# Performance work log

Measured on AMD Instinct MI355X. Metric: run time of the kernel, lower is better.

## Reference

```python
import jax, jax.numpy as jnp
import numpy as np

N = 10000        # nodes
E = 160000       # active edges
NS = 128         # scalar (0e) channels per tensor
NV = 64          # vector (1o) channels per tensor
LAT = 64         # latent dim
AVG_NEIGH = 16.0
SQ2 = float(np.sqrt(2.0))
SQ3 = float(np.sqrt(3.0))
EPS = 1e-5


def setup_inputs() -> dict:
    key = jax.random.key(0)
    ks = jax.random.split(key, 24)
    rn = lambda k, s: jax.random.normal(k, s, jnp.float32)
    d = {}
    d["latents"] = rn(ks[0], (E, LAT))
    d["node_features"] = rn(ks[1], (N, NS + 3 * NV))
    d["edge_features"] = rn(ks[2], (E, NS + 3 * NV))
    d["edge_sh"] = rn(ks[3], (E, 4))
    d["edge_index"] = jax.random.randint(ks[4], (2, E), 0, N)
    d["atom_type"] = jax.random.randint(ks[5], (N,), 0, 10)
    d["active_edges"] = jnp.arange(E)
    # separable layer norm affine params (node and edge)
    d["g_s_n"] = jnp.ones((NS,), jnp.float32); d["b_s_n"] = jnp.zeros((NS,), jnp.float32)
    d["g_v_n"] = jnp.ones((NV,), jnp.float32)
    d["g_s_e"] = jnp.ones((NS,), jnp.float32); d["b_s_e"] = jnp.zeros((NS,), jnp.float32)
    d["g_v_e"] = jnp.ones((NV,), jnp.float32)
    # FullyConnectedTensorProduct weights (path-normalized init).
    # tp input: 2*NS scalars, 2*NV vectors; sh: 1 scalar + 1 vector;
    # tp output: NS+NV scalars (scalars+gates), NV vectors.
    nSt, nVt, nSo = 2 * NS, 2 * NV, NS + NV
    d["W_ss0"] = rn(ks[6], (nSt, nSo)) / np.sqrt(nSt * 2)
    d["W_vv0"] = rn(ks[7], (nVt, nSo)) / np.sqrt(nVt * 2)
    d["W_sv1"] = rn(ks[8], (nSt, NV)) / np.sqrt(nSt * 3)
    d["W_vs1"] = rn(ks[9], (nVt, NV)) / np.sqrt(nVt * 3)
    d["W_vv1"] = rn(ks[10], (nVt, NV)) / np.sqrt(nVt * 3)
    # lin_post (per-l channel mixing)
    d["Wp_s"] = rn(ks[11], (NS, NS)) / np.sqrt(NS)
    d["Wp_v"] = rn(ks[12], (NV, NV)) / np.sqrt(NV)
    # env_embed_mlps: single linear latent -> weight_numel (NS+NV channels)
    d["W_env"] = rn(ks[13], (LAT, NS + NV)) / np.sqrt(LAT)
    # linear_res
    d["Wr_s"] = rn(ks[14], (NS, NS)) / np.sqrt(NS)
    d["Wr_v"] = rn(ks[15], (NV, NV)) / np.sqrt(NV)
    return d


def _sep_ln(x, g_s, b_s, g_v):
    # separable layer norm: standard LN on scalars, RMS-of-norms on vectors
    s = x[:, :NS]
    v = x[:, NS:].reshape(-1, NV, 3)
    mu = s.mean(-1, keepdims=True)
    var = ((s - mu) ** 2).mean(-1, keepdims=True)
    s = (s - mu) * jax.lax.rsqrt(var + EPS) * g_s + b_s
    vn = jnp.mean(jnp.sum(v * v, -1), -1, keepdims=True)  # (B,1)
    v = v * jax.lax.rsqrt(vn + EPS)[:, :, None] * g_v[None, :, None]
    return s, v


def _forward(latents, node_features, edge_features, edge_sh, edge_index,
             atom_type, active_edges,
             g_s_n, b_s_n, g_v_n, g_s_e, b_s_e, g_v_e,
             W_ss0, W_vv0, W_sv1, W_vs1, W_vv1,
             Wp_s, Wp_v, W_env, Wr_s, Wr_v):
    ec = edge_index[0][active_edges]                      # (E,) center nodes
    ns, nv = _sep_ln(node_features, g_s_n, b_s_n, g_v_n)
    es, ev = _sep_ln(edge_features, g_s_e, b_s_e, g_v_e)
    S = jnp.concatenate([ns[ec], es], axis=-1)            # (E, 2*NS)
    V = jnp.concatenate([nv[ec], ev], axis=1)             # (E, 2*NV, 3)
    sh0 = edge_sh[:, :1]                                  # (E,1)
    sh1 = edge_sh[:, 1:]                                  # (E,3)
    # fully-connected tensor product (tp_in x sh -> gate input)
    dotV = jnp.einsum('ecd,ed->ec', V, sh1) / SQ3         # 1x1->0
    out0 = (S * sh0) @ W_ss0 + dotV @ W_vv0               # (E, NS+NV) scalars
    out_v = (S @ W_sv1)[:, :, None] * sh1[:, None, :]     # 0x1->1
    out_v = out_v + jnp.einsum('ecd,cf->efd', V, W_vs1) * sh0[:, :, None]  # 1x0->1
    cross = jnp.cross(V, sh1[:, None, :]) / SQ2           # 1x1->1
    out_v = out_v + jnp.einsum('ecd,cf->efd', cross, W_vv1)  # (E, NV, 3)
    # gate
    s = jax.nn.silu(out0[:, :NS])
    gates = jax.nn.sigmoid(out0[:, NS:])
    v = out_v * gates[:, :, None]
    # lin_post
    s = s @ Wp_s
    v = jnp.einsum('ecd,cf->efd', v, Wp_v)
    # env weights from latents (elementwise linear per channel)
    w = latents[active_edges] @ W_env                     # (E, NS+NV)
    s = s * w[:, :NS]
    v = v * w[:, NS:][:, :, None]
    msg = jnp.concatenate([s, v.reshape(-1, 3 * NV)], axis=-1)  # (E, 320)
    agg = jax.ops.segment_sum(msg, ec, num_segments=N)
    agg = agg * jnp.float32(1.0 / np.sqrt(AVG_NEIGH))
    # residual linear on raw node features
    rs = node_features[:, :NS] @ Wr_s
    rv = jnp.einsum('ncd,cf->nfd', node_features[:, NS:].reshape(-1, NV, 3), Wr_v)
    res = jnp.concatenate([rs, rv.reshape(-1, 3 * NV)], axis=-1)
    return res + agg


def reference(latents, node_features, edge_features, edge_sh, edge_index,
              atom_type, active_edges,
              g_s_n, b_s_n, g_v_n, g_s_e, b_s_e, g_v_e,
              W_ss0, W_vv0, W_sv1, W_vs1, W_vv1,
              Wp_s, Wp_v, W_env, Wr_s, Wr_v):
    return _forward(latents, node_features, edge_features, edge_sh, edge_index,
                    atom_type, active_edges,
                    g_s_n, b_s_n, g_v_n, g_s_e, b_s_e, g_v_e,
                    W_ss0, W_vv0, W_sv1, W_vs1, W_vv1,
                    Wp_s, Wp_v, W_env, Wr_s, Wr_v)
```

## Files before the change

kernel.cpp:

```cpp
#include <hip/hip_runtime.h>

#define N_NODES 10000
#define N_EDGES 160000
#define NSC 128
#define ROW 320
#define EPS_LN 1e-5f
#define INV_SQ2 0.70710678118654752440f
#define INV_SQ3 0.57735026918962576451f

typedef unsigned short bfraw;
typedef __attribute__((ext_vector_type(8))) short short8;
typedef __attribute__((ext_vector_type(4))) float float4x;
typedef __attribute__((ext_vector_type(2))) float float2x;

__device__ __forceinline__ float bf2f(bfraw u) {
    union { unsigned int i; float f; } x; x.i = ((unsigned int)u) << 16; return x.f;
}
__device__ __forceinline__ bfraw f2bf(float f) {
    union { float f; unsigned int i; } x; x.f = f;
    unsigned int i = x.i;
    unsigned int lsb = (i >> 16) & 1u;
    i += 0x7fffu + lsb;
    return (bfraw)(i >> 16);
}
__device__ __forceinline__ unsigned cvt_pk_bf16(float lo, float hi) {
    unsigned r;
    asm("v_cvt_pk_bf16_f32 %0, %1, %2" : "=v"(r) : "v"(lo), "v"(hi));
    return r;
}
template<bool B> __device__ __forceinline__ float LD(const void* p, size_t i) {
    if (B) return bf2f(((const bfraw*)p)[i]);
    else   return ((const float*)p)[i];
}
template<bool B> __device__ __forceinline__ void ST(void* p, size_t i, float v) {
    if (B) ((bfraw*)p)[i] = f2bf(v);
    else   ((float*)p)[i] = v;
}
template<bool B> __device__ __forceinline__ float2x LD2(const void* p, size_t i) {
    float2x r;
    if (B) {
        unsigned u = *(const unsigned*)((const bfraw*)p + i);
        r.x = bf2f((bfraw)(u & 0xffffu)); r.y = bf2f((bfraw)(u >> 16));
    } else {
        r = *(const float2x*)((const float*)p + i);
    }
    return r;
}
template<bool B> __device__ __forceinline__ float4x LD4(const void* p, size_t i) {
    float4x r;
    if (B) {
        unsigned long long u = *(const unsigned long long*)((const bfraw*)p + i);
        r.x = bf2f((bfraw)(u & 0xffffu));
        r.y = bf2f((bfraw)((u >> 16) & 0xffffu));
        r.z = bf2f((bfraw)((u >> 32) & 0xffffu));
        r.w = bf2f((bfraw)(u >> 48));
    } else {
        r = *(const float4x*)((const float*)p + i);
    }
    return r;
}
__device__ __forceinline__ float wred64(float v) {
#pragma unroll
    for (int o = 32; o > 0; o >>= 1) v += __shfl_xor(v, o, 64);
    return v;
}
__device__ __forceinline__ void wredx12(float a[12]) {
#pragma unroll
    for (int o = 32; o > 0; o >>= 1) {
        float t[12];
#pragma unroll
        for (int i = 0; i < 12; i++) t[i] = __shfl_xor(a[i], o, 64);
#pragma unroll
        for (int i = 0; i < 12; i++) a[i] += t[i];
    }
}
__device__ __forceinline__ float silu_f(float x) { return x / (1.0f + __expf(-x)); }
__device__ __forceinline__ float sigm_f(float x) { return 1.0f / (1.0f + __expf(-x)); }

#define MFMA16(a, b, c) __builtin_amdgcn_mfma_f32_16x16x32_bf16((a), (b), (c), 0, 0, 0)

__device__ __forceinline__ int SDI(int r, int c) { return r * 384 + (c ^ ((r & 7) << 3)); }
__device__ __forceinline__ int X64(int r, int c) { return r * 64  + (c ^ ((r & 7) << 3)); }
__device__ __forceinline__ int SPI(int r, int c) { return r * 128 + (c ^ ((r & 7) << 3)); }
__device__ __forceinline__ int WVI(int r, int c) { return r * 192 + (c ^ ((r & 7) << 2)); }

__device__ __forceinline__ int dtype_flag(const void* g_s_n) {
    return (((const unsigned int*)g_s_n)[0] == 0x3F803F80u) ? 1 : 0;
}

__device__ __forceinline__ void pack_body(int idx, int fl,
    const void* Wss0, const void* Wvv0, const void* Wsv1, const void* Wvs1,
    const void* Wvv1, const void* Wps,  const void* Wpv,  const void* Wenv,
    const void* Wrs,  const void* Wrv,  bfraw* __restrict__ dst)
{
    const void* src; int K, N, base;
    if      (idx <  49152) { src = Wss0; K = 256; N = 192; base = 0; }
    else if (idx <  73728) { src = Wvv0; K = 128; N = 192; base = 49152; }
    else if (idx <  90112) { src = Wsv1; K = 256; N =  64; base = 73728; }
    else if (idx <  98304) { src = Wvs1; K = 128; N =  64; base = 90112; }
    else if (idx < 106496) { src = Wvv1; K = 128; N =  64; base = 98304; }
    else if (idx < 122880) { src = Wps;  K = 128; N = 128; base = 106496; }
    else if (idx < 126976) { src = Wpv;  K =  64; N =  64; base = 122880; }
    else if (idx < 139264) { src = Wenv; K =  64; N = 192; base = 126976; }
    else if (idx < 155648) { src = Wrs;  K = 128; N = 128; base = 139264; }
    else                   { src = Wrv;  K =  64; N =  64; base = 155648; }
    int li = idx - base;
    int j = li & 7, l = (li >> 3) & 63, t = li >> 9;
    int NT = N >> 4;
    int nt = t % NT, kt = t / NT;
    int k = kt * 32 + ((l >> 4) << 3) + j;
    int n = (nt << 4) + (l & 15);
    float v = fl ? bf2f(((const bfraw*)src)[(size_t)k * N + n])
                 : ((const float*)src)[(size_t)k * N + n];
    dst[idx] = f2bf(v);
}

template<bool B>
__device__ __forceinline__ void node_ln_body(int n, int lane,
    const void* nf, const void* g_s, const void* b_s, const void* g_v,
    bfraw* __restrict__ nsnv)
{
    size_t base = (size_t)n * ROW;
    float2x s = LD2<B>(nf, base + 2 * lane);
    float mu = wred64(s.x + s.y) * (1.0f / 128.0f);
    float m2 = wred64(s.x * s.x + s.y * s.y) * (1.0f / 128.0f);
    float rs = rsqrtf(m2 - mu * mu + EPS_LN);
    float2x g = LD2<B>(g_s, 2 * lane), b = LD2<B>(b_s, 2 * lane);
    float o0 = (s.x - mu) * rs * g.x + b.x;
    float o1 = (s.y - mu) * rs * g.y + b.y;
    float vx = LD<B>(nf, base + NSC + 3 * lane);
    float vy = LD<B>(nf, base + NSC + 3 * lane + 1);
    float vz = LD<B>(nf, base + NSC + 3 * lane + 2);
    float vn = wred64(vx * vx + vy * vy + vz * vz) * (1.0f / 64.0f);
    float rv = rsqrtf(vn + EPS_LN) * LD<B>(g_v, lane);
    bfraw* row = nsnv + (size_t)n * 320;
    ((unsigned*)row)[lane] = cvt_pk_bf16(o0, o1);
    row[128 + lane] = f2bf(vx * rv);
    row[192 + lane] = f2bf(vy * rv);
    row[256 + lane] = f2bf(vz * rv);
}

__global__ __launch_bounds__(256) void prep_k(
    const void* Wss0, const void* Wvv0, const void* Wsv1, const void* Wvs1,
    const void* Wvv1, const void* Wps,  const void* Wpv,  const void* Wenv,
    const void* Wrs,  const void* Wrv,  bfraw* __restrict__ pk,
    const int* __restrict__ eidx, const int* __restrict__ act, int* __restrict__ counts,
    const void* nf, const void* g_s_n, const void* b_s_n, const void* g_v_n,
    bfraw* __restrict__ nsnv)
{
    int fl = dtype_flag(g_s_n);
    int idx = blockIdx.x * 256 + threadIdx.x;
    if (idx < 159744)
        pack_body(idx, fl, Wss0, Wvv0, Wsv1, Wvs1, Wvv1, Wps, Wpv, Wenv, Wrs, Wrv, pk);
    if (idx < N_EDGES)
        atomicAdd(&counts[eidx[act[idx]]], 1);
    int w = threadIdx.x >> 6, lane = threadIdx.x & 63;
    int n = blockIdx.x * 4 + w;
    if (fl) node_ln_body<true >(n, lane, nf, g_s_n, b_s_n, g_v_n, nsnv);
    else    node_ln_body<false>(n, lane, nf, g_s_n, b_s_n, g_v_n, nsnv);
}

__global__ __launch_bounds__(1024) void scan_k(const int* __restrict__ counts,
                                               int* __restrict__ starts) {
    __shared__ int wsum[16];
    int t = threadIdx.x;
    int lo = t * 10;
    int lanev = t & 63, wv = t >> 6;
    int c[10];
    int s = 0;
    if (lo < N_NODES) {
#pragma unroll
        for (int j = 0; j < 10; j++) { c[j] = counts[lo + j]; s += c[j]; }
    }
    int ps = s;
#pragma unroll
    for (int o = 1; o < 64; o <<= 1) {
        int u = __shfl_up(ps, o, 64);
        if (lanev >= o) ps += u;
    }
    if (lanev == 63) wsum[wv] = ps;
    __syncthreads();
    if (t == 0) {
        int acc = 0;
#pragma unroll
        for (int i = 0; i < 16; i++) { int v = wsum[i]; wsum[i] = acc; acc += v; }
        starts[N_NODES] = acc;
    }
    __syncthreads();
    if (lo < N_NODES) {
        int acc = wsum[wv] + ps - s;
#pragma unroll
        for (int j = 0; j < 10; j++) { starts[lo + j] = acc; acc += c[j]; }
    }
}

__global__ void fill_k(const int* __restrict__ eidx, const int* __restrict__ act,
                       const int* __restrict__ starts, int* __restrict__ cursor,
                       int* __restrict__ inv) {
    int e = blockIdx.x * 256 + threadIdx.x;
    if (e < N_EDGES) {
        int n = eidx[act[e]];
        int pos = atomicAdd(&cursor[n], 1);
        inv[e] = starts[n] + pos;
    }
}

template<bool B>
__device__ void edge_body(char* smem, int tid,
    const bfraw* __restrict__ nsnv,
    const void* ef, const void* esh,
    const int* __restrict__ eidx, const int* __restrict__ act,
    const int* __restrict__ inv,
    const void* lat,
    const void* g_s_e, const void* b_s_e, const void* g_v_e,
    const bfraw* __restrict__ pk,
    bfraw* __restrict__ msg)
{
    bfraw* SD     = (bfraw*)(smem);
    bfraw* Vn     = (bfraw*)(smem + 12288);
    bfraw* Ve     = (bfraw*)(smem + 18432);
    bfraw* gate_u = (bfraw*)(smem + 18432);
    bfraw* sp_u   = (bfraw*)(smem + 20480);
    bfraw* lat_u  = (bfraw*)(smem + 24576);
    float* sh_f   = (float*)(smem + 26624);
    int*   slot_s = (int*)(smem + 26880);
    float* wenv_f = (float*)(smem);

    const bfraw* pWss0 = pk;
    const bfraw* pWvv0 = pk + 49152;
    const bfraw* pWsv1 = pk + 73728;
    const bfraw* pWvs1 = pk + 90112;
    const bfraw* pWvv1 = pk + 98304;
    const bfraw* pWps  = pk + 106496;
    const bfraw* pWpv  = pk + 122880;
    const bfraw* pWenv = pk + 126976;

    const int w = tid >> 6, lane = tid & 63;
    const int nl = lane & 15, mq = lane >> 4;
    const int e0 = blockIdx.x * 16;

    float2x gse = LD2<B>(g_s_e, 2 * lane), bse = LD2<B>(b_s_e, 2 * lane);
    float gve  = LD<B>(g_v_e, lane);

    int ae_[4], cn_[4], sl_[4];
#pragma unroll
    for (int i = 0; i < 4; i++) { ae_[i] = act[e0 + w * 4 + i]; sl_[i] = inv[e0 + w * 4 + i]; }
#pragma unroll
    for (int i = 0; i < 4; i++) cn_[i] = eidx[ae_[i]];

    float es0[4], es1[4], ex[4], ey[4], ez[4];
    float shv[4][4];
#pragma unroll
    for (int i = 0; i < 4; i++) {
        int el = w * 4 + i, e = e0 + el;
        float4x sh = LD4<B>(esh, (size_t)e * 4);
        shv[i][0] = sh.x; shv[i][1] = sh.y; shv[i][2] = sh.z; shv[i][3] = sh.w;
        size_t eb = (size_t)e * ROW;
        float2x es = LD2<B>(ef, eb + 2 * lane);
        es0[i] = es.x; es1[i] = es.y;
        ex[i]  = LD<B>(ef, eb + NSC + 3 * lane);
        ey[i]  = LD<B>(ef, eb + NSC + 3 * lane + 1);
        ez[i]  = LD<B>(ef, eb + NSC + 3 * lane + 2);
        const bfraw* nr = nsnv + (size_t)cn_[i] * 320;
        unsigned nsp = ((const unsigned*)nr)[lane];
        bfraw nvx = nr[128 + lane], nvy = nr[192 + lane], nvz = nr[256 + lane];
        float nx = bf2f(nvx), ny = bf2f(nvy), nz = bf2f(nvz);
        *(unsigned*)&SD[SDI(el, 2 * lane)] = nsp;
        SD[SDI(el, 256 + lane)] = f2bf((nx * sh.y + ny * sh.z + nz * sh.w) * INV_SQ3);
        Vn[X64(el, lane)]      = nvx;
        Vn[X64(16 + el, lane)] = nvy;
        Vn[X64(32 + el, lane)] = nvz;
        if (lane < 32) {
            float2x la = LD2<B>(lat, (size_t)ae_[i] * 64 + 2 * lane);
            *(unsigned*)&lat_u[X64(el, 2 * lane)] = cvt_pk_bf16(la.x, la.y);
        }
        if (lane == 0) {
            sh_f[el * 4]     = sh.x; sh_f[el * 4 + 1] = sh.y;
            sh_f[el * 4 + 2] = sh.z; sh_f[el * 4 + 3] = sh.w;
            slot_s[el] = sl_[i];
        }
    }
    float red[12];
#pragma unroll
    for (int i = 0; i < 4; i++) {
        red[i]     = es0[i] + es1[i];
        red[4 + i] = es0[i] * es0[i] + es1[i] * es1[i];
        red[8 + i] = ex[i] * ex[i] + ey[i] * ey[i] + ez[i] * ez[i];
    }
    wredx12(red);
#pragma unroll
    for (int i = 0; i < 4; i++) {
        int el = w * 4 + i;
        float mu  = red[i] * (1.0f / 128.0f);
        float var = red[4 + i] * (1.0f / 128.0f) - mu * mu;
        float rs  = rsqrtf(var + EPS_LN);
        float o0  = (es0[i] - mu) * rs * gse.x + bse.x;
        float o1  = (es1[i] - mu) * rs * gse.y + bse.y;
        float rv  = rsqrtf(red[8 + i] * (1.0f / 64.0f) + EPS_LN) * gve;
        float exn = ex[i] * rv, eyn = ey[i] * rv, ezn = ez[i] * rv;
        *(unsigned*)&SD[SDI(el, 128 + 2 * lane)] = cvt_pk_bf16(o0, o1);
        SD[SDI(el, 320 + lane)] = f2bf((exn * shv[i][1] + eyn * shv[i][2] + ezn * shv[i][3]) * INV_SQ3);
        Ve[X64(el, lane)]       = f2bf(exn);
        Ve[X64(16 + el, lane)]  = f2bf(eyn);
        Ve[X64(32 + el, lane)]  = f2bf(ezn);
    }
    __syncthreads();

    float4x sA0={0,0,0,0}, sA1={0,0,0,0}, sA2={0,0,0,0}, cSV={0,0,0,0};
    {
        const bfraw* ps = pWss0 + (size_t)(3 * w * 64 + lane) * 8;
        const bfraw* pv = pWsv1 + (size_t)(w * 64 + lane) * 8;
        short8 b0[4], b1[4];
#define LDG1(kt, D) do { \
        D[0] = *(const short8*)(ps + (kt) * 6144);        \
        D[1] = *(const short8*)(ps + (kt) * 6144 + 512);  \
        D[2] = *(const short8*)(ps + (kt) * 6144 + 1024); \
        D[3] = *(const short8*)(pv + (kt) * 2048); } while (0)
        LDG1(0, b0); LDG1(1, b1);
#pragma unroll
        for (int kt = 0; kt < 8; kt++) {
            short8 a = *(const short8*)&SD[SDI(nl, kt * 32 + mq * 8)];
            if ((kt & 1) == 0) {
                sA0 = MFMA16(a, b0[0], sA0); sA1 = MFMA16(a, b0[1], sA1);
                sA2 = MFMA16(a, b0[2], sA2); cSV = MFMA16(a, b0[3], cSV);
                if (kt + 2 < 8) LDG1(kt + 2, b0);
            } else {
                sA0 = MFMA16(a, b1[0], sA0); sA1 = MFMA16(a, b1[1], sA1);
                sA2 = MFMA16(a, b1[2], sA2); cSV = MFMA16(a, b1[3], cSV);
                if (kt + 2 < 8) LDG1(kt + 2, b1);
            }
        }
#undef LDG1
    }
    float4x dA0={0,0,0,0}, dA1={0,0,0,0}, dA2={0,0,0,0};
    {
        const bfraw* pd = pWvv0 + (size_t)(3 * w * 64 + lane) * 8;
        short8 c0[3], c1[3];
#define LDGD(kt, D) do { \
        D[0] = *(const short8*)(pd + (kt) * 6144);        \
        D[1] = *(const short8*)(pd + (kt) * 6144 + 512);  \
        D[2] = *(const short8*)(pd + (kt) * 6144 + 1024); } while (0)
        LDGD(0, c0); LDGD(1, c1);
#pragma unroll
        for (int kt = 0; kt < 4; kt++) {
            short8 a = *(const short8*)&SD[SDI(nl, 256 + kt * 32 + mq * 8)];
            if ((kt & 1) == 0) {
                dA0 = MFMA16(a, c0[0], dA0); dA1 = MFMA16(a, c0[1], dA1); dA2 = MFMA16(a, c0[2], dA2);
                if (kt + 2 < 4) LDGD(kt + 2, c0);
            } else {
                dA0 = MFMA16(a, c1[0], dA0); dA1 = MFMA16(a, c1[1], dA1); dA2 = MFMA16(a, c1[2], dA2);
                if (kt + 2 < 4) LDGD(kt + 2, c1);
            }
        }
#undef LDGD
    }
    float o_g1[3][4];
#pragma unroll
    for (int r = 0; r < 4; r++) {
        float sh0 = sh_f[(mq * 4 + r) * 4];
        o_g1[0][r] = sh0 * sA0[r] + dA0[r];
        o_g1[1][r] = sh0 * sA1[r] + dA1[r];
        o_g1[2][r] = sh0 * sA2[r] + dA2[r];
    }
    float4x H[3] = {{0,0,0,0},{0,0,0,0},{0,0,0,0}};
    float4x K[3] = {{0,0,0,0},{0,0,0,0},{0,0,0,0}};
    {
        const bfraw* ph = pWvs1 + (size_t)(w * 64 + lane) * 8;
        const bfraw* pq = pWvv1 + (size_t)(w * 64 + lane) * 8;
        short8 gH0 = *(const short8*)(ph);
        short8 gH1 = *(const short8*)(ph + 2048);
        short8 gH2 = *(const short8*)(ph + 4096);
        short8 gH3 = *(const short8*)(ph + 6144);
        short8 gK0 = *(const short8*)(pq);
        short8 gK1 = *(const short8*)(pq + 2048);
        short8 gK2 = *(const short8*)(pq + 4096);
        short8 gK3 = *(const short8*)(pq + 6144);
#pragma unroll
        for (int d = 0; d < 3; d++) {
            short8 a0 = *(const short8*)&Vn[X64(d * 16 + nl, mq * 8)];
            short8 a1 = *(const short8*)&Vn[X64(d * 16 + nl, 32 + mq * 8)];
            short8 a2 = *(const short8*)&Ve[X64(d * 16 + nl, mq * 8)];
            short8 a3 = *(const short8*)&Ve[X64(d * 16 + nl, 32 + mq * 8)];
            H[d] = MFMA16(a0, gH0, H[d]); K[d] = MFMA16(a0, gK0, K[d]);
            H[d] = MFMA16(a1, gH1, H[d]); K[d] = MFMA16(a1, gK1, K[d]);
            H[d] = MFMA16(a2, gH2, H[d]); K[d] = MFMA16(a2, gK2, K[d]);
            H[d] = MFMA16(a3, gH3, H[d]); K[d] = MFMA16(a3, gK3, K[d]);
        }
    }
    __syncthreads();

#pragma unroll
    for (int t = 0; t < 3; t++) {
        int tile = 3 * w + t;
#pragma unroll
        for (int r = 0; r < 4; r++) {
            int el = mq * 4 + r;
            float o = o_g1[t][r];
            if (tile < 8) sp_u[SPI(el, tile * 16 + nl)]         = f2bf(silu_f(o));
            else          gate_u[X64(el, (tile - 8) * 16 + nl)] = f2bf(sigm_f(o));
        }
    }
    __syncthreads();

    {
        int f = w * 16 + nl;
#pragma unroll
        for (int r = 0; r < 4; r++) {
            int el = mq * 4 + r;
            float g   = bf2f(gate_u[X64(el, f)]);
            float svv = cSV[r];
            float s0v = sh_f[el * 4], b0 = sh_f[el * 4 + 1], b1 = sh_f[el * 4 + 2], b2 = sh_f[el * 4 + 3];
            float ov0 = svv * b0 + s0v * H[0][r] + (b2 * K[1][r] - b1 * K[2][r]) * INV_SQ2;
            float ov1 = svv * b1 + s0v * H[1][r] + (b0 * K[2][r] - b2 * K[0][r]) * INV_SQ2;
            float ov2 = svv * b2 + s0v * H[2][r] + (b1 * K[0][r] - b0 * K[1][r]) * INV_SQ2;
            Vn[X64(el, f)]      = f2bf(ov0 * g);
            Vn[X64(16 + el, f)] = f2bf(ov1 * g);
            Vn[X64(32 + el, f)] = f2bf(ov2 * g);
        }
    }
    __syncthreads();

    float4x s2_0 = {0,0,0,0}, s2_1 = {0,0,0,0};
    {
        const bfraw* pp = pWps + (size_t)(w * 64 + lane) * 8;
        short8 u0[2], u1[2];
#define LDS2(kt, D) do { \
        D[0] = *(const short8*)(pp + (kt) * 4096);         \
        D[1] = *(const short8*)(pp + (kt) * 4096 + 2048); } while (0)
        LDS2(0, u0); LDS2(1, u1);
#pragma unroll
        for (int kt = 0; kt < 4; kt++) {
            short8 a = *(const short8*)&sp_u[SPI(nl, kt * 32 + mq * 8)];
            if ((kt & 1) == 0) {
                s2_0 = MFMA16(a, u0[0], s2_0); s2_1 = MFMA16(a, u0[1], s2_1);
                if (kt + 2 < 4) LDS2(kt + 2, u0);
            } else {
                s2_0 = MFMA16(a, u1[0], s2_0); s2_1 = MFMA16(a, u1[1], s2_1);
                if (kt + 2 < 4) LDS2(kt + 2, u1);
            }
        }
#undef LDS2
    }
    float4x wv0 = {0,0,0,0}, wv1 = {0,0,0,0}, wv2 = {0,0,0,0};
    {
        const bfraw* pe = pWenv + (size_t)(3 * w * 64 + lane) * 8;
        short8 e00 = *(const short8*)(pe);
        short8 e01 = *(const short8*)(pe + 512);
        short8 e02 = *(const short8*)(pe + 1024);
        short8 e10 = *(const short8*)(pe + 6144);
        short8 e11 = *(const short8*)(pe + 6144 + 512);
        short8 e12 = *(const short8*)(pe + 6144 + 1024);
        short8 a0 = *(const short8*)&lat_u[X64(nl, mq * 8)];
        short8 a1 = *(const short8*)&lat_u[X64(nl, 32 + mq * 8)];
        wv0 = MFMA16(a0, e00, wv0); wv0 = MFMA16(a1, e10, wv0);
        wv1 = MFMA16(a0, e01, wv1); wv1 = MFMA16(a1, e11, wv1);
        wv2 = MFMA16(a0, e02, wv2); wv2 = MFMA16(a1, e12, wv2);
    }
    float4x v2[3] = {{0,0,0,0},{0,0,0,0},{0,0,0,0}};
    {
        const bfraw* pz = pWpv + (size_t)(w * 64 + lane) * 8;
        short8 z0 = *(const short8*)(pz);
        short8 z1 = *(const short8*)(pz + 2048);
#pragma unroll
        for (int d = 0; d < 3; d++) {
            short8 a0 = *(const short8*)&Vn[X64(d * 16 + nl, mq * 8)];
            short8 a1 = *(const short8*)&Vn[X64(d * 16 + nl, 32 + mq * 8)];
            v2[d] = MFMA16(a0, z0, v2[d]);
            v2[d] = MFMA16(a1, z1, v2[d]);
        }
    }
    {
        float4x wvv[3] = {wv0, wv1, wv2};
#pragma unroll
        for (int t = 0; t < 3; t++)
#pragma unroll
            for (int r = 0; r < 4; r++)
                wenv_f[WVI(mq * 4 + r, (3 * w + t) * 16 + nl)] = wvv[t][r];
    }
    __syncthreads();

    int mslot[4];
#pragma unroll
    for (int r = 0; r < 4; r++) mslot[r] = slot_s[mq * 4 + r];
#pragma unroll
    for (int t = 0; t < 2; t++) {
        int c = (w + 4 * t) * 16 + nl;
        float4x s2v = (t == 0) ? s2_0 : s2_1;
#pragma unroll
        for (int r = 0; r < 4; r++) {
            int el = mq * 4 + r;
            msg[(size_t)mslot[r] * 320 + c] = f2bf(s2v[r] * wenv_f[WVI(el, c)]);
        }
    }
    {
        int f = w * 16 + nl;
#pragma unroll
        for (int r = 0; r < 4; r++) {
            int el = mq * 4 + r;
            float we = wenv_f[WVI(el, 128 + f)];
            size_t base = (size_t)mslot[r] * 320 + NSC + 3 * f;
            msg[base]     = f2bf(v2[0][r] * we);
            msg[base + 1] = f2bf(v2[1][r] * we);
            msg[base + 2] = f2bf(v2[2][r] * we);
        }
    }
}

__global__ __launch_bounds__(256, 6) void edge_mfma_k(
    const bfraw* __restrict__ nsnv,
    const void* ef, const void* esh,
    const int* __restrict__ eidx, const int* __restrict__ act,
    const int* __restrict__ inv,
    const void* lat,
    const void* g_s_e, const void* b_s_e, const void* g_v_e,
    const bfraw* __restrict__ pk,
    bfraw* __restrict__ msg, const void* g_s_n)
{
    __shared__ __align__(16) char smem[26944];
    if (dtype_flag(g_s_n))
        edge_body<true >(smem, threadIdx.x, nsnv, ef, esh, eidx, act, inv, lat,
                         g_s_e, b_s_e, g_v_e, pk, msg);
    else
        edge_body<false>(smem, threadIdx.x, nsnv, ef, esh, eidx, act, inv, lat,
                         g_s_e, b_s_e, g_v_e, pk, msg);
}

__device__ __forceinline__ float lo16(unsigned u) { return bf2f((bfraw)(u & 0xffffu)); }
__device__ __forceinline__ float hi16(unsigned u) { return bf2f((bfraw)(u >> 16)); }

__global__ __launch_bounds__(256) void gather_k(
    const bfraw* __restrict__ msg, const int* __restrict__ starts,
    float* __restrict__ agg)
{
    int w = threadIdx.x >> 6, lane = threadIdx.x & 63;
    int n = blockIdx.x * 4 + w;
    if (n >= N_NODES) return;
    int s0 = starts[n], s1 = starts[n + 1];
    bool half = lane < 32;
    float l0 = 0, h0 = 0, l1 = 0, h1 = 0, l2 = 0, h2 = 0;
    const unsigned* p = (const unsigned*)msg + (size_t)s0 * 160;
    int cnt = s1 - s0;
    int i = 0;
    for (; i + 3 < cnt; i += 4) {
        const unsigned* r0 = p + (size_t)i * 160;
        const unsigned* r1 = r0 + 160;
        const unsigned* r2 = r0 + 320;
        const unsigned* r3 = r0 + 480;
        unsigned a0 = r0[lane], b0 = r0[64 + lane];
        unsigned a1 = r1[lane], b1 = r1[64 + lane];
        unsigned a2 = r2[lane], b2 = r2[64 + lane];
        unsigned a3 = r3[lane], b3 = r3[64 + lane];
        unsigned c0 = half ? r0[128 + lane] : 0u;
        unsigned c1 = half ? r1[128 + lane] : 0u;
        unsigned c2 = half ? r2[128 + lane] : 0u;
        unsigned c3 = half ? r3[128 + lane] : 0u;
        l0 += (lo16(a0) + lo16(a1)) + (lo16(a2) + lo16(a3));
        h0 += (hi16(a0) + hi16(a1)) + (hi16(a2) + hi16(a3));
        l1 += (lo16(b0) + lo16(b1)) + (lo16(b2) + lo16(b3));
        h1 += (hi16(b0) + hi16(b1)) + (hi16(b2) + hi16(b3));
        l2 += (lo16(c0) + lo16(c1)) + (lo16(c2) + lo16(c3));
        h2 += (hi16(c0) + hi16(c1)) + (hi16(c2) + hi16(c3));
    }
    for (; i < cnt; i++) {
        const unsigned* r = p + (size_t)i * 160;
        unsigned a = r[lane], b = r[64 + lane];
        unsigned c = half ? r[128 + lane] : 0u;
        l0 += lo16(a); h0 += hi16(a);
        l1 += lo16(b); h1 += hi16(b);
        l2 += lo16(c); h2 += hi16(c);
    }
    float* o = agg + (size_t)n * ROW;
    float2x v0 = {l0, h0}, v1 = {l1, h1}, v2 = {l2, h2};
    ((float2x*)o)[lane] = v0;
    ((float2x*)(o + 128))[lane] = v1;
    if (half) ((float2x*)(o + 256))[lane] = v2;
}

template<bool B>
__device__ void final_body(char* smem, int tid,
    const void* nf, const float* __restrict__ agg,
    const bfraw* __restrict__ pk, void* out)
{
    bfraw* Sn_u = (bfraw*)(smem);
    bfraw* Vn_u = (bfraw*)(smem + 8704);
    const bfraw* pWrs = pk + 139264;
    const bfraw* pWrv = pk + 155648;

    const int w = tid >> 6, lane = tid & 63;
    const int nl = lane & 15, mq = lane >> 4;
    const int n0b = blockIdx.x * 32;

    for (int i = 0; i < 8; i++) {
        int el = w * 8 + i;
        int n = n0b + el;
        bool ok = n < N_NODES;
        size_t base = (size_t)n * ROW;
        float a0 = ok ? LD<B>(nf, base + lane) : 0.0f;
        float a1 = ok ? LD<B>(nf, base + 64 + lane) : 0.0f;
        float vx = ok ? LD<B>(nf, base + NSC + 3 * lane) : 0.0f;
        float vy = ok ? LD<B>(nf, base + NSC + 3 * lane + 1) : 0.0f;
        float vz = ok ? LD<B>(nf, base + NSC + 3 * lane + 2) : 0.0f;
        Sn_u[el * 136 + lane]      = f2bf(a0);
        Sn_u[el * 136 + 64 + lane] = f2bf(a1);
        Vn_u[(el) * 72 + lane]      = f2bf(vx);
        Vn_u[(32 + el) * 72 + lane] = f2bf(vy);
        Vn_u[(64 + el) * 72 + lane] = f2bf(vz);
    }
    __syncthreads();

    {
        const int mt = w & 1, ntb = (w >> 1) * 4;
        float4x c[4] = {{0,0,0,0},{0,0,0,0},{0,0,0,0},{0,0,0,0}};
#pragma unroll
        for (int kt = 0; kt < 4; kt++) {
            short8 a = *(const short8*)&Sn_u[(mt * 16 + nl) * 136 + kt * 32 + mq * 8];
#pragma unroll
            for (int t = 0; t < 4; t++) {
                short8 b = *(const short8*)&pWrs[((kt * 8 + ntb + t) * 64 + lane) * 8];
                c[t] = MFMA16(a, b, c[t]);
            }
        }
#pragma unroll
        for (int t = 0; t < 4; t++) {
            int cc = (ntb + t) * 16 + nl;
#pragma unroll
            for (int r = 0; r < 4; r++) {
                int n = n0b + mt * 16 + mq * 4 + r;
                if (n < N_NODES) {
                    size_t o = (size_t)n * ROW + cc;
                    ST<B>(out, o, c[t][r] + 0.25f * agg[o]);
                }
            }
        }
    }
    {
        float4x c[3][2] = {{{0,0,0,0},{0,0,0,0}},{{0,0,0,0},{0,0,0,0}},{{0,0,0,0},{0,0,0,0}}};
#pragma unroll
        for (int d = 0; d < 3; d++)
#pragma unroll
            for (int h = 0; h < 2; h++)
#pragma unroll
                for (int kt = 0; kt < 2; kt++) {
                    short8 a = *(const short8*)&Vn_u[(d * 32 + h * 16 + nl) * 72 + kt * 32 + mq * 8];
                    short8 b = *(const short8*)&pWrv[((kt * 4 + w) * 64 + lane) * 8];
                    c[d][h] = MFMA16(a, b, c[d][h]);
                }
        int f = w * 16 + nl;
#pragma unroll
        for (int h = 0; h < 2; h++)
#pragma unroll
            for (int r = 0; r < 4; r++) {
                int n = n0b + h * 16 + mq * 4 + r;
                if (n < N_NODES) {
                    size_t o = (size_t)n * ROW + NSC + 3 * f;
                    ST<B>(out, o,     c[0][h][r] + 0.25f * agg[o]);
                    ST<B>(out, o + 1, c[1][h][r] + 0.25f * agg[o + 1]);
                    ST<B>(out, o + 2, c[2][h][r] + 0.25f * agg[o + 2]);
                }
            }
    }
}

__global__ __launch_bounds__(256) void final_mfma_k(
    const void* nf, const float* __restrict__ agg,
    const bfraw* __restrict__ pk, void* out, const void* g_s_n)
{
    __shared__ __align__(16) char smem[22528];
    if (dtype_flag(g_s_n)) final_body<true >(smem, threadIdx.x, nf, agg, pk, out);
    else                   final_body<false>(smem, threadIdx.x, nf, agg, pk, out);
}

extern "C" void kernel_launch(void* const* d_in, const int* in_sizes, int n_in,
                              void* d_out, int out_size, void* d_ws, size_t ws_size,
                              hipStream_t stream)
{
    const void* latents = d_in[0];
    const void* node_f  = d_in[1];
    const void* edge_f  = d_in[2];
    const void* edge_sh = d_in[3];
    const int* edge_index = (const int*)d_in[4];
    const int* active     = (const int*)d_in[6];
    const void* g_s_n = d_in[7];
    const void* b_s_n = d_in[8];
    const void* g_v_n = d_in[9];
    const void* g_s_e = d_in[10];
    const void* b_s_e = d_in[11];
    const void* g_v_e = d_in[12];

    char* ws = (char*)d_ws;
    float* agg    = (float*)(ws + 256);
    bfraw* nsnv   = (bfraw*)(ws + 12800256);
    bfraw* pk     = (bfraw*)(ws + 25600256);
    int*   counts = (int*)(ws + 25919744);
    int*   cursor = (int*)(ws + 25960704);
    int*   starts = (int*)(ws + 26001664);
    int*   inv    = (int*)(ws + 26042624);
    bfraw* msg    = (bfraw*)(ws + 26682624);

    hipMemsetAsync(counts, 0, 81920, stream);
    prep_k<<<2500, 256, 0, stream>>>(d_in[13], d_in[14], d_in[15], d_in[16],
        d_in[17], d_in[18], d_in[19], d_in[20], d_in[21], d_in[22], pk,
        edge_index, active, counts, node_f, g_s_n, b_s_n, g_v_n, nsnv);
    scan_k<<<1, 1024, 0, stream>>>(counts, starts);
    fill_k<<<625, 256, 0, stream>>>(edge_index, active, starts, cursor, inv);
    edge_mfma_k<<<N_EDGES / 16, 256, 0, stream>>>(nsnv, edge_f, edge_sh, edge_index, active,
        inv, latents, g_s_e, b_s_e, g_v_e, pk, msg, g_s_n);
    gather_k<<<N_NODES / 4, 256, 0, stream>>>(msg, starts, agg);
    final_mfma_k<<<(N_NODES + 31) / 32, 256, 0, stream>>>(node_f, agg, pk, (void*)d_out, g_s_n);
}
```

Measured before the change: 602.2 us.

## Iterate edges in CSR order and fuse gather into final residual kernel

The fill kernel now writes a CSR permutation (slot -> edge) instead of an inverse map, so the edge kernel reads edges in sorted-by-destination order and writes messages contiguously to its own slot range instead of scattering rows. The separate gather kernel is removed: the final kernel sums each node's message rows into a shared-memory aggregate and adds it to the residual linear, which avoids the fp32 agg round trip through global memory and one launch. In exchange, edge-input reads become indirect gathers, and the final kernel uses about 64KB of LDS per block with 32 nodes per block, which lowers occupancy and parallelism for the gather phase.

```diff
diff --git a/kernel.cpp b/kernel.cpp
--- a/kernel.cpp
+++ b/kernel.cpp
@@ -196,12 +196,12 @@
 
 __global__ void fill_k(const int* __restrict__ eidx, const int* __restrict__ act,
                        const int* __restrict__ starts, int* __restrict__ cursor,
-                       int* __restrict__ inv) {
+                       int* __restrict__ csr) {
     int e = blockIdx.x * 256 + threadIdx.x;
     if (e < N_EDGES) {
         int n = eidx[act[e]];
         int pos = atomicAdd(&cursor[n], 1);
-        inv[e] = starts[n] + pos;
+        csr[starts[n] + pos] = e;
     }
 }
 
@@ -210,7 +210,7 @@
     const bfraw* __restrict__ nsnv,
     const void* ef, const void* esh,
     const int* __restrict__ eidx, const int* __restrict__ act,
-    const int* __restrict__ inv,
+    const int* __restrict__ csr,
     const void* lat,
     const void* g_s_e, const void* b_s_e, const void* g_v_e,
     const bfraw* __restrict__ pk,
@@ -223,7 +223,6 @@
     bfraw* sp_u   = (bfraw*)(smem + 20480);
     bfraw* lat_u  = (bfraw*)(smem + 24576);
     float* sh_f   = (float*)(smem + 26624);
-    int*   slot_s = (int*)(smem + 26880);
     float* wenv_f = (float*)(smem);
 
     const bfraw* pWss0 = pk;
@@ -237,14 +236,16 @@
 
     const int w = tid >> 6, lane = tid & 63;
     const int nl = lane & 15, mq = lane >> 4;
-    const int e0 = blockIdx.x * 16;
+    const int s0b = blockIdx.x * 16;
 
     float2x gse = LD2<B>(g_s_e, 2 * lane), bse = LD2<B>(b_s_e, 2 * lane);
     float gve  = LD<B>(g_v_e, lane);
 
-    int ae_[4], cn_[4], sl_[4];
-#pragma unroll
-    for (int i = 0; i < 4; i++) { ae_[i] = act[e0 + w * 4 + i]; sl_[i] = inv[e0 + w * 4 + i]; }
+    int e_[4], ae_[4], cn_[4];
+#pragma unroll
+    for (int i = 0; i < 4; i++) e_[i] = csr[s0b + w * 4 + i];
+#pragma unroll
+    for (int i = 0; i < 4; i++) ae_[i] = act[e_[i]];
 #pragma unroll
     for (int i = 0; i < 4; i++) cn_[i] = eidx[ae_[i]];
 
@@ -252,7 +253,8 @@
     float shv[4][4];
 #pragma unroll
     for (int i = 0; i < 4; i++) {
-        int el = w * 4 + i, e = e0 + el;
+        int el = w * 4 + i;
+        int e = e_[i];
         float4x sh = LD4<B>(esh, (size_t)e * 4);
         shv[i][0] = sh.x; shv[i][1] = sh.y; shv[i][2] = sh.z; shv[i][3] = sh.w;
         size_t eb = (size_t)e * ROW;
@@ -277,7 +279,6 @@
         if (lane == 0) {
             sh_f[el * 4]     = sh.x; sh_f[el * 4 + 1] = sh.y;
             sh_f[el * 4 + 2] = sh.z; sh_f[el * 4 + 3] = sh.w;
-            slot_s[el] = sl_[i];
         }
     }
     float red[12];
@@ -479,9 +480,6 @@
     }
     __syncthreads();
 
-    int mslot[4];
-#pragma unroll
-    for (int r = 0; r < 4; r++) mslot[r] = slot_s[mq * 4 + r];
 #pragma unroll
     for (int t = 0; t < 2; t++) {
         int c = (w + 4 * t) * 16 + nl;
@@ -489,7 +487,7 @@
 #pragma unroll
         for (int r = 0; r < 4; r++) {
             int el = mq * 4 + r;
-            msg[(size_t)mslot[r] * 320 + c] = f2bf(s2v[r] * wenv_f[WVI(el, c)]);
+            msg[(size_t)(s0b + el) * 320 + c] = f2bf(s2v[r] * wenv_f[WVI(el, c)]);
         }
     }
     {
@@ -498,7 +496,7 @@
         for (int r = 0; r < 4; r++) {
             int el = mq * 4 + r;
             float we = wenv_f[WVI(el, 128 + f)];
-            size_t base = (size_t)mslot[r] * 320 + NSC + 3 * f;
+            size_t base = (size_t)(s0b + el) * 320 + NSC + 3 * f;
             msg[base]     = f2bf(v2[0][r] * we);
             msg[base + 1] = f2bf(v2[1][r] * we);
             msg[base + 2] = f2bf(v2[2][r] * we);
@@ -510,79 +508,33 @@
     const bfraw* __restrict__ nsnv,
     const void* ef, const void* esh,
     const int* __restrict__ eidx, const int* __restrict__ act,
-    const int* __restrict__ inv,
+    const int* __restrict__ csr,
     const void* lat,
     const void* g_s_e, const void* b_s_e, const void* g_v_e,
     const bfraw* __restrict__ pk,
     bfraw* __restrict__ msg, const void* g_s_n)
 {
-    __shared__ __align__(16) char smem[26944];
+    __shared__ __align__(16) char smem[26880];
     if (dtype_flag(g_s_n))
-        edge_body<true >(smem, threadIdx.x, nsnv, ef, esh, eidx, act, inv, lat,
+        edge_body<true >(smem, threadIdx.x, nsnv, ef, esh, eidx, act, csr, lat,
                          g_s_e, b_s_e, g_v_e, pk, msg);
     else
-        edge_body<false>(smem, threadIdx.x, nsnv, ef, esh, eidx, act, inv, lat,
+        edge_body<false>(smem, threadIdx.x, nsnv, ef, esh, eidx, act, csr, lat,
                          g_s_e, b_s_e, g_v_e, pk, msg);
 }
 
 __device__ __forceinline__ float lo16(unsigned u) { return bf2f((bfraw)(u & 0xffffu)); }
 __device__ __forceinline__ float hi16(unsigned u) { return bf2f((bfraw)(u >> 16)); }
-
-__global__ __launch_bounds__(256) void gather_k(
-    const bfraw* __restrict__ msg, const int* __restrict__ starts,
-    float* __restrict__ agg)
-{
-    int w = threadIdx.x >> 6, lane = threadIdx.x & 63;
-    int n = blockIdx.x * 4 + w;
-    if (n >= N_NODES) return;
-    int s0 = starts[n], s1 = starts[n + 1];
-    bool half = lane < 32;
-    float l0 = 0, h0 = 0, l1 = 0, h1 = 0, l2 = 0, h2 = 0;
-    const unsigned* p = (const unsigned*)msg + (size_t)s0 * 160;
-    int cnt = s1 - s0;
-    int i = 0;
-    for (; i + 3 < cnt; i += 4) {
-        const unsigned* r0 = p + (size_t)i * 160;
-        const unsigned* r1 = r0 + 160;
-        const unsigned* r2 = r0 + 320;
-        const unsigned* r3 = r0 + 480;
-        unsigned a0 = r0[lane], b0 = r0[64 + lane];
-        unsigned a1 = r1[lane], b1 = r1[64 + lane];
-        unsigned a2 = r2[lane], b2 = r2[64 + lane];
-        unsigned a3 = r3[lane], b3 = r3[64 + lane];
-        unsigned c0 = half ? r0[128 + lane] : 0u;
-        unsigned c1 = half ? r1[128 + lane] : 0u;
-        unsigned c2 = half ? r2[128 + lane] : 0u;
-        unsigned c3 = half ? r3[128 + lane] : 0u;
-        l0 += (lo16(a0) + lo16(a1)) + (lo16(a2) + lo16(a3));
-        h0 += (hi16(a0) + hi16(a1)) + (hi16(a2) + hi16(a3));
-        l1 += (lo16(b0) + lo16(b1)) + (lo16(b2) + lo16(b3));
-        h1 += (hi16(b0) + hi16(b1)) + (hi16(b2) + hi16(b3));
-        l2 += (lo16(c0) + lo16(c1)) + (lo16(c2) + lo16(c3));
-        h2 += (hi16(c0) + hi16(c1)) + (hi16(c2) + hi16(c3));
-    }
-    for (; i < cnt; i++) {
-        const unsigned* r = p + (size_t)i * 160;
-        unsigned a = r[lane], b = r[64 + lane];
-        unsigned c = half ? r[128 + lane] : 0u;
-        l0 += lo16(a); h0 += hi16(a);
-        l1 += lo16(b); h1 += hi16(b);
-        l2 += lo16(c); h2 += hi16(c);
-    }
-    float* o = agg + (size_t)n * ROW;
-    float2x v0 = {l0, h0}, v1 = {l1, h1}, v2 = {l2, h2};
-    ((float2x*)o)[lane] = v0;
-    ((float2x*)(o + 128))[lane] = v1;
-    if (half) ((float2x*)(o + 256))[lane] = v2;
-}
+#define AGP 324
 
 template<bool B>
 __device__ void final_body(char* smem, int tid,
-    const void* nf, const float* __restrict__ agg,
-    const bfraw* __restrict__ pk, void* out)
+    const bfraw* __restrict__ msg, const int* __restrict__ starts,
+    const void* nf, const bfraw* __restrict__ pk, void* out)
 {
-    bfraw* Sn_u = (bfraw*)(smem);
-    bfraw* Vn_u = (bfraw*)(smem + 8704);
+    float* agg_f = (float*)(smem);
+    bfraw* Sn_u  = (bfraw*)(smem + 41472);
+    bfraw* Vn_u  = (bfraw*)(smem + 41472 + 8704);
     const bfraw* pWrs = pk + 139264;
     const bfraw* pWrv = pk + 155648;
 
@@ -606,6 +558,50 @@
         Vn_u[(32 + el) * 72 + lane] = f2bf(vy);
         Vn_u[(64 + el) * 72 + lane] = f2bf(vz);
     }
+
+    bool half = lane < 32;
+    for (int i = 0; i < 8; i++) {
+        int el = w * 8 + i;
+        int n = n0b + el;
+        if (n >= N_NODES) break;
+        int s0 = starts[n], s1 = starts[n + 1];
+        float l0 = 0, h0 = 0, l1 = 0, h1 = 0, l2 = 0, h2 = 0;
+        const unsigned* p = (const unsigned*)msg + (size_t)s0 * 160;
+        int cnt = s1 - s0;
+        int j = 0;
+        for (; j + 3 < cnt; j += 4) {
+            const unsigned* r0 = p + (size_t)j * 160;
+            const unsigned* r1 = r0 + 160;
+            const unsigned* r2 = r0 + 320;
+            const unsigned* r3 = r0 + 480;
+            unsigned a0 = r0[lane], b0 = r0[64 + lane];
+            unsigned a1 = r1[lane], b1 = r1[64 + lane];
+            unsigned a2 = r2[lane], b2 = r2[64 + lane];
+            unsigned a3 = r3[lane], b3 = r3[64 + lane];
+            unsigned c0 = half ? r0[128 + lane] : 0u;
+            unsigned c1 = half ? r1[128 + lane] : 0u;
+            unsigned c2 = half ? r2[128 + lane] : 0u;
+            unsigned c3 = half ? r3[128 + lane] : 0u;
+            l0 += (lo16(a0) + lo16(a1)) + (lo16(a2) + lo16(a3));
+            h0 += (hi16(a0) + hi16(a1)) + (hi16(a2) + hi16(a3));
+            l1 += (lo16(b0) + lo16(b1)) + (lo16(b2) + lo16(b3));
+            h1 += (hi16(b0) + hi16(b1)) + (hi16(b2) + hi16(b3));
+            l2 += (lo16(c0) + lo16(c1)) + (lo16(c2) + lo16(c3));
+            h2 += (hi16(c0) + hi16(c1)) + (hi16(c2) + hi16(c3));
+        }
+        for (; j < cnt; j++) {
+            const unsigned* r = p + (size_t)j * 160;
+            unsigned a = r[lane], b = r[64 + lane];
+            unsigned c = half ? r[128 + lane] : 0u;
+            l0 += lo16(a); h0 += hi16(a);
+            l1 += lo16(b); h1 += hi16(b);
+            l2 += lo16(c); h2 += hi16(c);
+        }
+        float* o = agg_f + el * AGP;
+        o[2 * lane] = l0;      o[2 * lane + 1] = h0;
+        o[128 + 2 * lane] = l1; o[128 + 2 * lane + 1] = h1;
+        if (half) { o[256 + 2 * lane] = l2; o[256 + 2 * lane + 1] = h2; }
+    }
     __syncthreads();
 
     {
@@ -625,10 +621,10 @@
             int cc = (ntb + t) * 16 + nl;
 #pragma unroll
             for (int r = 0; r < 4; r++) {
-                int n = n0b + mt * 16 + mq * 4 + r;
+                int el = mt * 16 + mq * 4 + r;
+                int n = n0b + el;
                 if (n < N_NODES) {
-                    size_t o = (size_t)n * ROW + cc;
-                    ST<B>(out, o, c[t][r] + 0.25f * agg[o]);
+                    ST<B>(out, (size_t)n * ROW + cc, c[t][r] + 0.25f * agg_f[el * AGP + cc]);
                 }
             }
         }
@@ -650,24 +646,26 @@
         for (int h = 0; h < 2; h++)
 #pragma unroll
             for (int r = 0; r < 4; r++) {
-                int n = n0b + h * 16 + mq * 4 + r;
+                int el = h * 16 + mq * 4 + r;
+                int n = n0b + el;
                 if (n < N_NODES) {
                     size_t o = (size_t)n * ROW + NSC + 3 * f;
-                    ST<B>(out, o,     c[0][h][r] + 0.25f * agg[o]);
-                    ST<B>(out, o + 1, c[1][h][r] + 0.25f * agg[o + 1]);
-                    ST<B>(out, o + 2, c[2][h][r] + 0.25f * agg[o + 2]);
+                    const float* ag = agg_f + el * AGP + 128 + 3 * f;
+                    ST<B>(out, o,     c[0][h][r] + 0.25f * ag[0]);
+                    ST<B>(out, o + 1, c[1][h][r] + 0.25f * ag[1]);
+                    ST<B>(out, o + 2, c[2][h][r] + 0.25f * ag[2]);
                 }
             }
     }
 }
 
-__global__ __launch_bounds__(256) void final_mfma_k(
-    const void* nf, const float* __restrict__ agg,
-    const bfraw* __restrict__ pk, void* out, const void* g_s_n)
+__global__ __launch_bounds__(256) void final_gather_k(
+    const bfraw* __restrict__ msg, const int* __restrict__ starts,
+    const void* nf, const bfraw* __restrict__ pk, void* out, const void* g_s_n)
 {
-    __shared__ __align__(16) char smem[22528];
-    if (dtype_flag(g_s_n)) final_body<true >(smem, threadIdx.x, nf, agg, pk, out);
-    else                   final_body<false>(smem, threadIdx.x, nf, agg, pk, out);
+    __shared__ __align__(16) char smem[64000];
+    if (dtype_flag(g_s_n)) final_body<true >(smem, threadIdx.x, msg, starts, nf, pk, out);
+    else                   final_body<false>(smem, threadIdx.x, msg, starts, nf, pk, out);
 }
 
 extern "C" void kernel_launch(void* const* d_in, const int* in_sizes, int n_in,
@@ -688,13 +686,12 @@
     const void* g_v_e = d_in[12];
 
     char* ws = (char*)d_ws;
-    float* agg    = (float*)(ws + 256);
     bfraw* nsnv   = (bfraw*)(ws + 12800256);
     bfraw* pk     = (bfraw*)(ws + 25600256);
     int*   counts = (int*)(ws + 25919744);
     int*   cursor = (int*)(ws + 25960704);
     int*   starts = (int*)(ws + 26001664);
-    int*   inv    = (int*)(ws + 26042624);
+    int*   csr    = (int*)(ws + 26042624);
     bfraw* msg    = (bfraw*)(ws + 26682624);
 
     hipMemsetAsync(counts, 0, 81920, stream);
@@ -702,9 +699,9 @@
         d_in[17], d_in[18], d_in[19], d_in[20], d_in[21], d_in[22], pk,
         edge_index, active, counts, node_f, g_s_n, b_s_n, g_v_n, nsnv);
     scan_k<<<1, 1024, 0, stream>>>(counts, starts);
-    fill_k<<<625, 256, 0, stream>>>(edge_index, active, starts, cursor, inv);
+    fill_k<<<625, 256, 0, stream>>>(edge_index, active, starts, cursor, csr);
     edge_mfma_k<<<N_EDGES / 16, 256, 0, stream>>>(nsnv, edge_f, edge_sh, edge_index, active,
-        inv, latents, g_s_e, b_s_e, g_v_e, pk, msg, g_s_n);
-    gather_k<<<N_NODES / 4, 256, 0, stream>>>(msg, starts, agg);
-    final_mfma_k<<<(N_NODES + 31) / 32, 256, 0, stream>>>(node_f, agg, pk, (void*)d_out, g_s_n);
-}
+        csr, latents, g_s_e, b_s_e, g_v_e, pk, msg, g_s_n);
+    final_gather_k<<<(N_NODES + 31) / 32, 256, 0, stream>>>(msg, starts, node_f, pk,
+        (void*)d_out, g_s_n);
+}
```

Result: slower. 639.9 us (+6.3%).
